# Performance work log

Hardware: AMD Instinct MI355X
Metric: run time of the kernel (lower is better)

The kernel has to match this reference:

```python
import jax, jax.numpy as jnp
import numpy as np

D_MODEL = 2048
NUM_HEADS = 16
D_K = D_MODEL // NUM_HEADS


def setup_inputs() -> dict:
    key = jax.random.key(0)
    ks = jax.random.split(key, 9)
    s = 1.0 / np.sqrt(D_MODEL)
    return {
        "x": jax.random.normal(ks[0], (2, 2048, D_MODEL), dtype=jnp.float32),
        "Wq": jax.random.normal(ks[1], (D_MODEL, D_MODEL), dtype=jnp.float32) * s,
        "bq": jax.random.normal(ks[2], (D_MODEL,), dtype=jnp.float32) * 0.01,
        "Wk": jax.random.normal(ks[3], (D_MODEL, D_MODEL), dtype=jnp.float32) * s,
        "bk": jax.random.normal(ks[4], (D_MODEL,), dtype=jnp.float32) * 0.01,
        "Wv": jax.random.normal(ks[5], (D_MODEL, D_MODEL), dtype=jnp.float32) * s,
        "bv": jax.random.normal(ks[6], (D_MODEL,), dtype=jnp.float32) * 0.01,
        "Wo": jax.random.normal(ks[7], (D_MODEL, D_MODEL), dtype=jnp.float32) * s,
        "bo": jax.random.normal(ks[8], (D_MODEL,), dtype=jnp.float32) * 0.01,
    }


def reference(x, Wq, bq, Wk, bk, Wv, bv, Wo, bo):
    B, T, C = x.shape
    H, Dk = NUM_HEADS, D_K
    # projections (torch Linear: y = x @ W^T + b; here weights stored as [in,out])
    q = (x @ Wq + bq).reshape(B, T, H, Dk).transpose(0, 2, 1, 3)  # [B,H,T,Dk]
    k = (x @ Wk + bk).reshape(B, T, H, Dk).transpose(0, 2, 1, 3)
    v = (x @ Wv + bv).reshape(B, T, H, Dk).transpose(0, 2, 1, 3)
    score = jnp.einsum("bhqd,bhkd->bhqk", q, k) / jnp.sqrt(jnp.float32(Dk))
    attn = jax.nn.softmax(score, axis=-1)
    out = jnp.einsum("bhqk,bhkd->bhqd", attn, v)  # [B,H,T,Dk]
    out = out.transpose(0, 2, 1, 3).reshape(B, T, C)
    return out @ Wo + bo
```

## Files before the change

kernel.cpp:

```cpp
#include <hip/hip_runtime.h>
#include <cstdint>

typedef _Float16 f16;
typedef __attribute__((ext_vector_type(4))) _Float16 f16x4;
typedef __attribute__((ext_vector_type(8))) _Float16 f16x8;
typedef __attribute__((ext_vector_type(4))) float f32x4;

#define DM   2048
#define TSEQ 2048
#define NB   2
#define NH   16
#define DKH  128
#define LOG2E 1.44269504088896f

__device__ __forceinline__ void gload_lds16(const void* g, void* l) {
  __builtin_amdgcn_global_load_lds((const __attribute__((address_space(1))) void*)g,
                                   (__attribute__((address_space(3))) void*)l, 16, 0, 0);
}

#define SBAR()  { asm volatile("s_barrier" ::: "memory"); __builtin_amdgcn_sched_barrier(0); }
#define LGKM0() { asm volatile("s_waitcnt lgkmcnt(0)" ::: "memory"); __builtin_amdgcn_sched_barrier(0); }
#define VMCNT0() { asm volatile("s_waitcnt vmcnt(0)" ::: "memory"); __builtin_amdgcn_sched_barrier(0); }

__global__ __launch_bounds__(256) void cvt_kernel(const float* __restrict__ src,
                                                  f16* __restrict__ dst, int n8) {
  int i = blockIdx.x * 256 + threadIdx.x;
  if (i >= n8) return;
  const float4* s = (const float4*)src + 2 * (size_t)i;
  float4 a = s[0], b = s[1];
  f16x8 o;
  o[0]=(f16)a.x; o[1]=(f16)a.y; o[2]=(f16)a.z; o[3]=(f16)a.w;
  o[4]=(f16)b.x; o[5]=(f16)b.y; o[6]=(f16)b.z; o[7]=(f16)b.w;
  ((f16x8*)dst)[i] = o;
}

__global__ __launch_bounds__(256) void wt_kernel(const float* __restrict__ W0, const float* __restrict__ W1,
                                                 const float* __restrict__ W2, const float* __restrict__ W3,
                                                 f16* __restrict__ Dqkv, f16* __restrict__ Dout) {
  __shared__ f16 S[64 * 80];
  int z = blockIdx.z;
  const float* W = (z == 0) ? W0 : (z == 1) ? W1 : (z == 2) ? W2 : W3;
  f16* D = (z < 3) ? (Dqkv + (size_t)z * DM * DM) : Dout;
  int n0 = blockIdx.x * 64, k0 = blockIdx.y * 64;
  int tid = threadIdx.x;
#pragma unroll
  for (int i = 0; i < 4; i++) {
    int flat = i * 256 + tid;
    int r = flat >> 4, c4 = flat & 15;
    float4 v = *(const float4*)(W + (size_t)(k0 + r) * DM + n0 + c4 * 4);
    S[(c4 * 4 + 0) * 80 + r] = (f16)v.x;
    S[(c4 * 4 + 1) * 80 + r] = (f16)v.y;
    S[(c4 * 4 + 2) * 80 + r] = (f16)v.z;
    S[(c4 * 4 + 3) * 80 + r] = (f16)v.w;
  }
  __syncthreads();
#pragma unroll
  for (int i = 0; i < 2; i++) {
    int flat = i * 256 + tid;
    int nl = flat >> 3, kc = flat & 7;
    f16x8 v = *(const f16x8*)&S[nl * 80 + kc * 8];
    *(f16x8*)(D + (size_t)(n0 + nl) * DM + k0 + kc * 8) = v;
  }
}

template <int MODE>
__global__ __launch_bounds__(512, 2) void gemm_kernel(const f16* __restrict__ A, const f16* __restrict__ Bt,
                                                      const float* __restrict__ b0, const float* __restrict__ b1,
                                                      const float* __restrict__ b2,
                                                      f16* __restrict__ Oh, float* __restrict__ Of) {
  constexpr int BN   = (MODE == 0) ? 192 : 128;
  constexpr int NFR  = BN / 64;
  constexpr int WN   = BN / 4;
  constexpr int NXB  = (MODE == 0) ? 32 : 16;
  constexpr int CPX  = (16 * NXB) / 8;
  constexpr int UNITS = 4 + NFR;
  __shared__ __align__(16) f16 As[2][256 * 64];
  __shared__ __align__(16) f16 Bs[2][NFR * 64 * 64];
  const int K = DM;
  const int NT = K / 64;
  const int NITER = NT / 2;
  int tid = threadIdx.x, l = tid & 63, w = tid >> 6;
  int lo = l & 15, hi = l >> 4;
  int wm = w >> 2, wn = w & 3;
  int lin = blockIdx.x;
  int swz = (lin & 7) * CPX + (lin >> 3);
  int by = swz & 15, bx = swz >> 4;
  int m0 = by * 256, n0 = bx * BN;

  const f16* Ag = A + (size_t)m0 * K;
  const f16* Bg = Bt + (size_t)n0 * K;

  auto stageAu = [&](int b, int u, int t) {
    int rin = (w << 3) + (l >> 3);
    int csw = (l & 7) ^ (rin & 7);
    gload_lds16(Ag + (size_t)(u * 64 + rin) * K + t * 64 + csw * 8,
                &As[b][u * 4096 + w * 512]);
  };
  auto stageBu = [&](int b, int u, int t) {
    int rin = (w << 3) + (l >> 3);
    int csw = (l & 7) ^ (rin & 7);
    gload_lds16(Bg + (size_t)(u * 64 + rin) * K + t * 64 + csw * 8,
                &Bs[b][u * 4096 + w * 512]);
  };
  auto stageAll = [&](int b, int t) {
#pragma unroll
    for (int u = 0; u < 4; u++) stageAu(b, u, t);
#pragma unroll
    for (int u = 0; u < NFR; u++) stageBu(b, u, t);
  };

  f32x4 acc[8][NFR] = {};
  f16x8 bfr[NFR][2];
  f16x8 af[4][2][2];

#define READ_BFR(b)                                                                 \
  {                                                                                 \
    _Pragma("unroll")                                                               \
    for (int ni = 0; ni < NFR; ni++) {                                              \
      int row = wn * WN + ni * 16 + lo;                                             \
      bfr[ni][0] = *(const f16x8*)&Bs[b][row * 64 + (((0 + hi) ^ (row & 7)) << 3)]; \
      bfr[ni][1] = *(const f16x8*)&Bs[b][row * 64 + (((4 + hi) ^ (row & 7)) << 3)]; \
    }                                                                               \
  }

#define READ_AF(b, q)                                                               \
  {                                                                                 \
    _Pragma("unroll")                                                               \
    for (int e = 0; e < 2; e++) {                                                   \
      int row = wm * 128 + ((q) * 2 + e) * 16 + lo;                                 \
      af[q][e][0] = *(const f16x8*)&As[b][row * 64 + (((0 + hi) ^ (row & 7)) << 3)]; \
      af[q][e][1] = *(const f16x8*)&As[b][row * 64 + (((4 + hi) ^ (row & 7)) << 3)]; \
    }                                                                               \
  }

#define MFMA_Q(q)                                                                   \
    __builtin_amdgcn_s_setprio(1);                                                  \
    _Pragma("unroll")                                                               \
    for (int e = 0; e < 2; e++)                                                     \
      _Pragma("unroll")                                                             \
      for (int ni = 0; ni < NFR; ni++) {                                            \
        acc[(q)*2+e][ni] = __builtin_amdgcn_mfma_f32_16x16x32_f16(af[q][e][0], bfr[ni][0], acc[(q)*2+e][ni], 0, 0, 0); \
        acc[(q)*2+e][ni] = __builtin_amdgcn_mfma_f32_16x16x32_f16(af[q][e][1], bfr[ni][1], acc[(q)*2+e][ni], 0, 0, 0); \
      }                                                                             \
    __builtin_amdgcn_s_setprio(0);

#define VMCNT_P()                                                                   \
    if constexpr (MODE == 0) { asm volatile("s_waitcnt vmcnt(7)" ::: "memory"); }   \
    else                     { asm volatile("s_waitcnt vmcnt(6)" ::: "memory"); }   \
    __builtin_amdgcn_sched_barrier(0);

  stageAll(0, 0);
  stageAll(1, 1);
  VMCNT_P();
  SBAR();
  READ_BFR(0); READ_AF(0, 0);

#pragma unroll 1
  for (int it = 0; it < NITER; ++it) {
    int t2 = (2 * it + 2 < NT) ? 2 * it + 2 : NT - 1;
    int t3 = (2 * it + 3 < NT) ? 2 * it + 3 : NT - 1;

    MFMA_Q(0); READ_AF(0, 1);
    MFMA_Q(1); READ_AF(0, 2);
    MFMA_Q(2); READ_AF(0, 3);
    LGKM0();
    VMCNT0();
    SBAR();
    stageAll(0, t2);
    MFMA_Q(3);
    __builtin_amdgcn_sched_barrier(0);
    READ_BFR(1); READ_AF(1, 0);

    MFMA_Q(0); READ_AF(1, 1);
    MFMA_Q(1); READ_AF(1, 2);
    MFMA_Q(2); READ_AF(1, 3);
    LGKM0();
    VMCNT0();
    SBAR();
    stageAll(1, t3);
    MFMA_Q(3);
    __builtin_amdgcn_sched_barrier(0);
    READ_BFR(0); READ_AF(0, 0);
  }
  asm volatile("s_waitcnt vmcnt(0) lgkmcnt(0)" ::: "memory");

#pragma unroll
  for (int mi = 0; mi < 8; mi++) {
    int gm = m0 + wm * 128 + mi * 16 + (hi << 2);
#pragma unroll
    for (int ni = 0; ni < NFR; ni++) {
      int gn = n0 + wn * WN + ni * 16 + lo;
      if (MODE == 0) {
        int proj = gn >> 11, nn = gn & 2047;
        const float* bp = (proj == 0) ? b0 : (proj == 1) ? b1 : b2;
        float bias = bp[nn];
        int h = nn >> 7, d = nn & 127;
        int b = gm >> 11;
        int t0 = gm & 2047;
        if (proj < 2) {
#pragma unroll
          for (int r = 0; r < 4; r++) {
            Oh[(size_t)proj * ((size_t)NB * NH * TSEQ * DKH) +
               (((size_t)(b * NH + h) * TSEQ + t0 + r) * DKH) + d] = (f16)(acc[mi][ni][r] + bias);
          }
        } else {
          f16x4 pk;
#pragma unroll
          for (int r = 0; r < 4; r++) pk[r] = (f16)(acc[mi][ni][r] + bias);
          *(f16x4*)(Oh + 2ull * ((size_t)NB * NH * TSEQ * DKH) +
                    ((size_t)(b * NH + h) * DKH + d) * TSEQ + t0) = pk;
        }
      } else {
        float bias = b0[gn];
#pragma unroll
        for (int r = 0; r < 4; r++)
          Of[(size_t)(gm + r) * DM + gn] = acc[mi][ni][r] + bias;
      }
    }
  }
#undef READ_BFR
#undef READ_AF
#undef MFMA_Q
#undef VMCNT_P
}

__global__ __launch_bounds__(256, 2) void attn_kernel(const f16* __restrict__ Qb, const f16* __restrict__ Kb,
                                                      const f16* __restrict__ Vtb, f16* __restrict__ AO) {
  __shared__ f16 Ks[64 * 128];
  __shared__ f16 Vt[128 * 64];
  __shared__ f16 Ps[4][32 * 72];
  int tid = threadIdx.x, l = tid & 63, w = tid >> 6;
  int lo = l & 15, hi = l >> 4;
  int lin = blockIdx.x;
  int xcd = lin & 7, slot = lin >> 3;
  int bh = xcd * 4 + (slot & 3), qt = slot >> 2;
  const float CSC = 0.12753257f;
  const float THR = 62.0f;
  const f16* Qg = Qb + (size_t)bh * TSEQ * DKH;
  const f16* Kg = Kb + (size_t)bh * TSEQ * DKH;
  const f16* Vg = Vtb + (size_t)bh * DKH * TSEQ;

  f16x8 aq[2][4];
#pragma unroll
  for (int hf = 0; hf < 2; hf++) {
    int qrow = qt * 128 + w * 32 + hf * 16 + lo;
#pragma unroll
    for (int c = 0; c < 4; c++)
      aq[hf][c] = *(const f16x8*)(Qg + (size_t)qrow * DKH + c * 32 + (hi << 3));
  }

  f32x4 o[2][8] = {};
  float mrow[2] = {-INFINITY, -INFINITY};
  float lrow[2] = {0.f, 0.f};

  for (int ktile = 0; ktile < TSEQ / 64; ++ktile) {
    __syncthreads();
#pragma unroll
    for (int i = 0; i < 4; i++) {
      int chunk = (w * 4 + i) * 64 + l;
      int rowk = chunk >> 4, c = chunk & 15;
      int csw = c ^ (rowk & 15);
      gload_lds16(Kg + (size_t)(ktile * 64 + rowk) * DKH + csw * 8, &Ks[(w * 4 + i) * 512]);
    }
#pragma unroll
    for (int i = 0; i < 4; i++) {
      int chunk = (w * 4 + i) * 64 + l;
      int d = chunk >> 3, c = chunk & 7;
      int csw = c ^ (d & 7);
      gload_lds16(Vg + (size_t)d * TSEQ + ktile * 64 + csw * 8, &Vt[(w * 4 + i) * 512]);
    }
    __syncthreads();

    f32x4 s[2][4] = {};
    __builtin_amdgcn_s_setprio(1);
#pragma unroll
    for (int ks = 0; ks < 4; ++ks) {
      int ktl = ks * 16 + lo;
#pragma unroll
      for (int c = 0; c < 4; c++) {
        int cc = (c * 4 + hi) ^ lo;
        f16x8 bk = *(const f16x8*)&Ks[ktl * 128 + cc * 8];
        s[0][ks] = __builtin_amdgcn_mfma_f32_16x16x32_f16(bk, aq[0][c], s[0][ks], 0, 0, 0);
        s[1][ks] = __builtin_amdgcn_mfma_f32_16x16x32_f16(bk, aq[1][c], s[1][ks], 0, 0, 0);
      }
    }
    __builtin_amdgcn_s_setprio(0);

#pragma unroll
    for (int hf = 0; hf < 2; hf++) {
      float mk[4];
#pragma unroll
      for (int ks = 0; ks < 4; ks++)
        mk[ks] = fmaxf(fmaxf(s[hf][ks][0], s[hf][ks][1]), fmaxf(s[hf][ks][2], s[hf][ks][3]));
      float mt = fmaxf(fmaxf(mk[0], mk[1]), fmaxf(mk[2], mk[3]));
      mt = fmaxf(mt, __shfl_xor(mt, 16));
      mt = fmaxf(mt, __shfl_xor(mt, 32));

      if (__any(mt > mrow[hf] + THR)) {
        float mn = fmaxf(mrow[hf], mt);
        float al = exp2f((mrow[hf] - mn) * CSC);
        mrow[hf] = mn;
        lrow[hf] *= al;
        float alr[4];
#pragma unroll
        for (int r = 0; r < 4; r++) alr[r] = __shfl(al, (hi << 2) + r);
#pragma unroll
        for (int dsub = 0; dsub < 8; dsub++)
#pragma unroll
          for (int r = 0; r < 4; r++) o[hf][dsub][r] *= alr[r];
      }

      float mCn = -mrow[hf] * CSC;
      float sum = 0.f;
#pragma unroll
      for (int ks = 0; ks < 4; ks++) {
        f16x4 pk;
        float part = 0.f;
#pragma unroll
        for (int r = 0; r < 4; r++) {
          float p = exp2f(__builtin_fmaf(s[hf][ks][r], CSC, mCn));
          pk[r] = (f16)p;
          part += p;
        }
        sum += part;
        *(f16x4*)&Ps[w][(hf * 16 + lo) * 72 + ks * 16 + (hi << 2)] = pk;
      }
      sum += __shfl_xor(sum, 16);
      sum += __shfl_xor(sum, 32);
      lrow[hf] += sum;
    }

    f16x8 pa[2][2];
#pragma unroll
    for (int hf = 0; hf < 2; hf++)
#pragma unroll
      for (int kk = 0; kk < 2; kk++)
        pa[hf][kk] = *(const f16x8*)&Ps[w][(hf * 16 + lo) * 72 + kk * 32 + (hi << 3)];
    __builtin_amdgcn_s_setprio(1);
#pragma unroll
    for (int kk = 0; kk < 2; kk++) {
#pragma unroll
      for (int dsub = 0; dsub < 8; dsub++) {
        int d = dsub * 16 + lo;
        f16x8 vf = *(const f16x8*)&Vt[d * 64 + (((kk * 4 + hi) ^ (d & 7)) << 3)];
        o[0][dsub] = __builtin_amdgcn_mfma_f32_16x16x32_f16(pa[0][kk], vf, o[0][dsub], 0, 0, 0);
        o[1][dsub] = __builtin_amdgcn_mfma_f32_16x16x32_f16(pa[1][kk], vf, o[1][dsub], 0, 0, 0);
      }
    }
    __builtin_amdgcn_s_setprio(0);
  }

  int b = bh >> 4, h = bh & 15;
#pragma unroll
  for (int hf = 0; hf < 2; hf++) {
    float inv = 1.0f / lrow[hf];
    float invr[4];
#pragma unroll
    for (int r = 0; r < 4; r++) invr[r] = __shfl(inv, (hi << 2) + r);
#pragma unroll
    for (int r = 0; r < 4; r++) {
      int t = qt * 128 + w * 32 + hf * 16 + (hi << 2) + r;
      f16* dst = AO + ((size_t)b * TSEQ + t) * DM + h * DKH;
#pragma unroll
      for (int dsub = 0; dsub < 8; dsub++)
        dst[dsub * 16 + lo] = (f16)(o[hf][dsub][r] * invr[r]);
    }
  }
}

extern "C" void kernel_launch(void* const* d_in, const int* in_sizes, int n_in,
                              void* d_out, int out_size, void* d_ws, size_t ws_size,
                              hipStream_t stream) {
  const float* x  = (const float*)d_in[0];
  const float* Wq = (const float*)d_in[1];
  const float* bq = (const float*)d_in[2];
  const float* Wk = (const float*)d_in[3];
  const float* bk = (const float*)d_in[4];
  const float* Wv = (const float*)d_in[5];
  const float* bv = (const float*)d_in[6];
  const float* Wo = (const float*)d_in[7];
  const float* bo = (const float*)d_in[8];

  f16* ws    = (f16*)d_ws;
  f16* xb    = ws;
  f16* WtQKV = ws + 8388608ull;
  f16* WtO   = ws + 20971520ull;
  f16* Q     = ws + 25165824ull;
  f16* Kp    = ws + 33554432ull;
  f16* Vp    = ws + 41943040ull;
  f16* AO    = xb;

  cvt_kernel<<<4096, 256, 0, stream>>>(x, xb, (NB * TSEQ * DM) / 8);
  wt_kernel<<<dim3(32, 32, 4), 256, 0, stream>>>(Wq, Wk, Wv, Wo, WtQKV, WtO);
  gemm_kernel<0><<<512, 512, 0, stream>>>(xb, WtQKV, bq, bk, bv, Q, nullptr);
  attn_kernel<<<512, 256, 0, stream>>>(Q, Kp, Vp, AO);
  gemm_kernel<1><<<256, 512, 0, stream>>>(AO, WtO, bo, nullptr, nullptr, nullptr, (float*)d_out);
}
```

Baseline: 261.9 us.

## Switch GEMM to 32x32x16 MFMA with 4x2 warp layout

Replaces the 16x16x32 MFMA tiling in the projection GEMMs with 32x32x16 MFMA instructions. The 8 waves are rearranged from a 2x4 to a 4x2 grid, each wave now computing a 64xWN tile with 32x32 fragments. All A and B fragments for a 64-wide K tile are now read up front instead of being interleaved with the MFMAs, and the epilogue is remapped to the 32x32 accumulator layout. The aim is fewer LDS reads per flop and denser matrix-core issue. The cost is more fragment registers live at once and less overlap between LDS reads and MFMAs.

```diff
diff --git a/kernel.cpp b/kernel.cpp
--- a/kernel.cpp
+++ b/kernel.cpp
@@ -5,6 +5,7 @@
 typedef __attribute__((ext_vector_type(4))) _Float16 f16x4;
 typedef __attribute__((ext_vector_type(8))) _Float16 f16x8;
 typedef __attribute__((ext_vector_type(4))) float f32x4;
+typedef __attribute__((ext_vector_type(16))) float f32x16;
 
 #define DM   2048
 #define TSEQ 2048
@@ -69,19 +70,19 @@
                                                       const float* __restrict__ b2,
                                                       f16* __restrict__ Oh, float* __restrict__ Of) {
   constexpr int BN   = (MODE == 0) ? 192 : 128;
-  constexpr int NFR  = BN / 64;
-  constexpr int WN   = BN / 4;
+  constexpr int NF2  = BN / 64;
+  constexpr int NU   = BN / 64;
+  constexpr int WN   = BN / 2;
   constexpr int NXB  = (MODE == 0) ? 32 : 16;
   constexpr int CPX  = (16 * NXB) / 8;
-  constexpr int UNITS = 4 + NFR;
   __shared__ __align__(16) f16 As[2][256 * 64];
-  __shared__ __align__(16) f16 Bs[2][NFR * 64 * 64];
+  __shared__ __align__(16) f16 Bs[2][NU * 64 * 64];
   const int K = DM;
   const int NT = K / 64;
   const int NITER = NT / 2;
   int tid = threadIdx.x, l = tid & 63, w = tid >> 6;
-  int lo = l & 15, hi = l >> 4;
-  int wm = w >> 2, wn = w & 3;
+  int l31 = l & 31, hi2 = l >> 5;
+  int wm = w >> 1, wn = w & 1;
   int lin = blockIdx.x;
   int swz = (lin & 7) * CPX + (lin >> 3);
   int by = swz & 15, bx = swz >> 4;
@@ -106,121 +107,124 @@
 #pragma unroll
     for (int u = 0; u < 4; u++) stageAu(b, u, t);
 #pragma unroll
-    for (int u = 0; u < NFR; u++) stageBu(b, u, t);
+    for (int u = 0; u < NU; u++) stageBu(b, u, t);
   };
 
-  f32x4 acc[8][NFR] = {};
-  f16x8 bfr[NFR][2];
-  f16x8 af[4][2][2];
-
-#define READ_BFR(b)                                                                 \
-  {                                                                                 \
-    _Pragma("unroll")                                                               \
-    for (int ni = 0; ni < NFR; ni++) {                                              \
-      int row = wn * WN + ni * 16 + lo;                                             \
-      bfr[ni][0] = *(const f16x8*)&Bs[b][row * 64 + (((0 + hi) ^ (row & 7)) << 3)]; \
-      bfr[ni][1] = *(const f16x8*)&Bs[b][row * 64 + (((4 + hi) ^ (row & 7)) << 3)]; \
-    }                                                                               \
-  }
-
-#define READ_AF(b, q)                                                               \
-  {                                                                                 \
-    _Pragma("unroll")                                                               \
-    for (int e = 0; e < 2; e++) {                                                   \
-      int row = wm * 128 + ((q) * 2 + e) * 16 + lo;                                 \
-      af[q][e][0] = *(const f16x8*)&As[b][row * 64 + (((0 + hi) ^ (row & 7)) << 3)]; \
-      af[q][e][1] = *(const f16x8*)&As[b][row * 64 + (((4 + hi) ^ (row & 7)) << 3)]; \
-    }                                                                               \
-  }
-
-#define MFMA_Q(q)                                                                   \
-    __builtin_amdgcn_s_setprio(1);                                                  \
-    _Pragma("unroll")                                                               \
-    for (int e = 0; e < 2; e++)                                                     \
-      _Pragma("unroll")                                                             \
-      for (int ni = 0; ni < NFR; ni++) {                                            \
-        acc[(q)*2+e][ni] = __builtin_amdgcn_mfma_f32_16x16x32_f16(af[q][e][0], bfr[ni][0], acc[(q)*2+e][ni], 0, 0, 0); \
-        acc[(q)*2+e][ni] = __builtin_amdgcn_mfma_f32_16x16x32_f16(af[q][e][1], bfr[ni][1], acc[(q)*2+e][ni], 0, 0, 0); \
-      }                                                                             \
+  f32x16 acc[2][NF2] = {};
+  f16x8 af[2][4];
+  f16x8 bfr[NF2][4];
+
+#define READ_BFR(b)                                                                  \
+  {                                                                                  \
+    _Pragma("unroll")                                                                \
+    for (int nf = 0; nf < NF2; nf++) {                                               \
+      int row = wn * WN + nf * 32 + l31;                                             \
+      _Pragma("unroll")                                                              \
+      for (int ks = 0; ks < 4; ks++)                                                 \
+        bfr[nf][ks] = *(const f16x8*)&Bs[b][row * 64 + (((ks * 2 + hi2) ^ (row & 7)) << 3)]; \
+    }                                                                                \
+  }
+
+#define READ_AF(b)                                                                   \
+  {                                                                                  \
+    _Pragma("unroll")                                                                \
+    for (int mf = 0; mf < 2; mf++) {                                                 \
+      int row = wm * 64 + mf * 32 + l31;                                             \
+      _Pragma("unroll")                                                              \
+      for (int ks = 0; ks < 4; ks++)                                                 \
+        af[mf][ks] = *(const f16x8*)&As[b][row * 64 + (((ks * 2 + hi2) ^ (row & 7)) << 3)]; \
+    }                                                                                \
+  }
+
+#define MFMA_KS(ks)                                                                  \
+    __builtin_amdgcn_s_setprio(1);                                                   \
+    _Pragma("unroll")                                                                \
+    for (int mf = 0; mf < 2; mf++)                                                   \
+      _Pragma("unroll")                                                              \
+      for (int nf = 0; nf < NF2; nf++)                                               \
+        acc[mf][nf] = __builtin_amdgcn_mfma_f32_32x32x16_f16(af[mf][ks], bfr[nf][ks], acc[mf][nf], 0, 0, 0); \
     __builtin_amdgcn_s_setprio(0);
 
-#define VMCNT_P()                                                                   \
-    if constexpr (MODE == 0) { asm volatile("s_waitcnt vmcnt(7)" ::: "memory"); }   \
-    else                     { asm volatile("s_waitcnt vmcnt(6)" ::: "memory"); }   \
+#define VMCNT_P()                                                                    \
+    if constexpr (MODE == 0) { asm volatile("s_waitcnt vmcnt(7)" ::: "memory"); }    \
+    else                     { asm volatile("s_waitcnt vmcnt(6)" ::: "memory"); }    \
     __builtin_amdgcn_sched_barrier(0);
 
   stageAll(0, 0);
   stageAll(1, 1);
   VMCNT_P();
   SBAR();
-  READ_BFR(0); READ_AF(0, 0);
+  READ_BFR(0); READ_AF(0);
 
 #pragma unroll 1
   for (int it = 0; it < NITER; ++it) {
     int t2 = (2 * it + 2 < NT) ? 2 * it + 2 : NT - 1;
     int t3 = (2 * it + 3 < NT) ? 2 * it + 3 : NT - 1;
 
-    MFMA_Q(0); READ_AF(0, 1);
-    MFMA_Q(1); READ_AF(0, 2);
-    MFMA_Q(2); READ_AF(0, 3);
+    MFMA_KS(0); MFMA_KS(1); MFMA_KS(2);
     LGKM0();
     VMCNT0();
     SBAR();
     stageAll(0, t2);
-    MFMA_Q(3);
+    MFMA_KS(3);
     __builtin_amdgcn_sched_barrier(0);
-    READ_BFR(1); READ_AF(1, 0);
-
-    MFMA_Q(0); READ_AF(1, 1);
-    MFMA_Q(1); READ_AF(1, 2);
-    MFMA_Q(2); READ_AF(1, 3);
+    READ_BFR(1); READ_AF(1);
+
+    MFMA_KS(0); MFMA_KS(1); MFMA_KS(2);
     LGKM0();
     VMCNT0();
     SBAR();
     stageAll(1, t3);
-    MFMA_Q(3);
+    MFMA_KS(3);
     __builtin_amdgcn_sched_barrier(0);
-    READ_BFR(0); READ_AF(0, 0);
+    READ_BFR(0); READ_AF(0);
   }
   asm volatile("s_waitcnt vmcnt(0) lgkmcnt(0)" ::: "memory");
 
 #pragma unroll
-  for (int mi = 0; mi < 8; mi++) {
-    int gm = m0 + wm * 128 + mi * 16 + (hi << 2);
-#pragma unroll
-    for (int ni = 0; ni < NFR; ni++) {
-      int gn = n0 + wn * WN + ni * 16 + lo;
+  for (int mf = 0; mf < 2; mf++) {
+#pragma unroll
+    for (int nf = 0; nf < NF2; nf++) {
+      int gn = n0 + wn * WN + nf * 32 + l31;
       if (MODE == 0) {
         int proj = gn >> 11, nn = gn & 2047;
         const float* bp = (proj == 0) ? b0 : (proj == 1) ? b1 : b2;
         float bias = bp[nn];
         int h = nn >> 7, d = nn & 127;
-        int b = gm >> 11;
-        int t0 = gm & 2047;
-        if (proj < 2) {
-#pragma unroll
-          for (int r = 0; r < 4; r++) {
-            Oh[(size_t)proj * ((size_t)NB * NH * TSEQ * DKH) +
-               (((size_t)(b * NH + h) * TSEQ + t0 + r) * DKH) + d] = (f16)(acc[mi][ni][r] + bias);
+#pragma unroll
+        for (int v = 0; v < 4; v++) {
+          int gm = m0 + wm * 64 + mf * 32 + v * 8 + hi2 * 4;
+          int b = gm >> 11;
+          int t0 = gm & 2047;
+          if (proj < 2) {
+#pragma unroll
+            for (int r = 0; r < 4; r++) {
+              Oh[(size_t)proj * ((size_t)NB * NH * TSEQ * DKH) +
+                 (((size_t)(b * NH + h) * TSEQ + t0 + r) * DKH) + d] = (f16)(acc[mf][nf][v * 4 + r] + bias);
+            }
+          } else {
+            f16x4 pk;
+#pragma unroll
+            for (int r = 0; r < 4; r++) pk[r] = (f16)(acc[mf][nf][v * 4 + r] + bias);
+            *(f16x4*)(Oh + 2ull * ((size_t)NB * NH * TSEQ * DKH) +
+                      ((size_t)(b * NH + h) * DKH + d) * TSEQ + t0) = pk;
           }
-        } else {
-          f16x4 pk;
-#pragma unroll
-          for (int r = 0; r < 4; r++) pk[r] = (f16)(acc[mi][ni][r] + bias);
-          *(f16x4*)(Oh + 2ull * ((size_t)NB * NH * TSEQ * DKH) +
-                    ((size_t)(b * NH + h) * DKH + d) * TSEQ + t0) = pk;
         }
       } else {
         float bias = b0[gn];
 #pragma unroll
-        for (int r = 0; r < 4; r++)
-          Of[(size_t)(gm + r) * DM + gn] = acc[mi][ni][r] + bias;
+        for (int v = 0; v < 4; v++) {
+          int gm = m0 + wm * 64 + mf * 32 + v * 8 + hi2 * 4;
+#pragma unroll
+          for (int r = 0; r < 4; r++)
+            Of[(size_t)(gm + r) * DM + gn] = acc[mf][nf][v * 4 + r] + bias;
+        }
       }
     }
   }
 #undef READ_BFR
 #undef READ_AF
-#undef MFMA_Q
+#undef MFMA_KS
 #undef VMCNT_P
 }
 
```

Measured after the change: 274.2 us. +4.7%, slower.
